# Optimization experiments

Hardware: AMD Instinct MI355X
Metric: run time of the kernel (lower is better)

## Reference

```python
import jax, jax.numpy as jnp
import numpy as np
import math

N_NODES = 20000
N_EDGES = 320000
DIM = 256
NUM_HEADS = 8


def setup_inputs() -> dict:
    key = jax.random.key(0)
    ks = jax.random.split(key, 8)
    x = jax.random.normal(ks[0], (N_NODES, DIM), dtype=jnp.float32)
    edge_index = jax.random.randint(ks[1], (2, N_EDGES), 0, N_NODES, dtype=jnp.int64)
    edge_attr = jax.random.normal(ks[2], (N_EDGES, DIM), dtype=jnp.float32)
    s = 1.0 / math.sqrt(DIM)
    Wq = jax.random.uniform(ks[3], (DIM, DIM), jnp.float32, -s, s)
    Wk = jax.random.uniform(ks[4], (DIM, DIM), jnp.float32, -s, s)
    Wv = jax.random.uniform(ks[5], (DIM, DIM), jnp.float32, -s, s)
    We = jax.random.uniform(ks[6], (DIM, DIM), jnp.float32, -s, s)
    be = jax.random.uniform(ks[7], (DIM,), jnp.float32, -s, s)
    return {"x": x, "edge_index": edge_index, "edge_attr": edge_attr,
            "Wq": Wq, "Wk": Wk, "Wv": Wv, "We": We, "be": be}


def reference(x, edge_index, edge_attr, Wq, Wk, Wv, We, be):
    N = x.shape[0]
    E = edge_attr.shape[0]
    H = NUM_HEADS
    C = DIM // H  # per-head channels (concat=True)
    src = edge_index[0]  # segment / attention-grouping index
    dst = edge_index[1]
    # Z = edge_attr * x[dst]  -> [E, D]
    Z = edge_attr * x[dst]
    q = x @ Wq.T          # [N, D]
    k = Z @ Wk.T          # [E, D]
    v = Z @ Wv.T          # [E, D]
    edge_out = Z @ We.T + be  # [E, D]
    # split heads
    qh = q.reshape(N, H, C)
    kh = k.reshape(E, H, C)
    vh = v.reshape(E, H, C)
    # per-edge, per-head score: sum(q[src]*k)/sqrt(C)   -> [E, H]
    scores = jnp.einsum('ehc,ehc->eh', qh[src], kh) / math.sqrt(C)
    # segment softmax grouped by src node
    m = jax.ops.segment_max(scores, src, num_segments=N)        # [N, H]
    ex = jnp.exp(scores - m[src])                               # [E, H]
    denom = jax.ops.segment_sum(ex, src, num_segments=N)        # [N, H]
    attn = ex / (denom[src] + 1e-16)                            # [E, H]
    # weighted scatter-sum of values -> [N, H, C] -> [N, D]
    out = jax.ops.segment_sum(attn[:, :, None] * vh, src, num_segments=N)
    out = out.reshape(N, H * C)
    return (out, edge_out)
```

## Files before the change

### kernel.cpp

```cpp
#include <hip/hip_runtime.h>
#include <math.h>

#define NN 20000
#define NE 320000
#define DIM 256

typedef __bf16 bf16x8 __attribute__((ext_vector_type(8)));
typedef float f32x4 __attribute__((ext_vector_type(4)));
typedef int i32x4 __attribute__((ext_vector_type(4)));
typedef unsigned short u16x4 __attribute__((ext_vector_type(4)));

union B8 { i32x4 i; bf16x8 b; };

__device__ __forceinline__ unsigned short f2bf(float f) {
  unsigned int u; __builtin_memcpy(&u, &f, 4);
  u += 0x7fffu + ((u >> 16) & 1u);
  return (unsigned short)(u >> 16);
}
__device__ __forceinline__ float bf2f(unsigned short h) {
  unsigned int u = ((unsigned int)h) << 16;
  float f; __builtin_memcpy(&f, &u, 4);
  return f;
}

__global__ __launch_bounds__(256) void pack_w(const float* __restrict__ W,
                                              unsigned short* __restrict__ wf) {
  int t = blockIdx.x * 256 + threadIdx.x;
  int lane = t & 63, ct = (t >> 6) & 15, ks = t >> 10;
  int col = ct * 16 + (lane & 15);
  int k0 = ks * 32 + (lane >> 4) * 8;
  const float* src = W + col * 256 + k0;
  unsigned int h[8];
#pragma unroll
  for (int j = 0; j < 8; j++) h[j] = f2bf(src[j]);
  i32x4 v;
  v.x = (int)(h[0] | (h[1] << 16));
  v.y = (int)(h[2] | (h[3] << 16));
  v.z = (int)(h[4] | (h[5] << 16));
  v.w = (int)(h[6] | (h[7] << 16));
  ((i32x4*)wf)[t] = v;
}

__device__ __forceinline__ void gemm_tile(const unsigned short* zs,
                                          const unsigned short* wf,
                                          int lane, int wv, f32x4 (&acc)[4][4]) {
#pragma unroll 1
  for (int ksI = 0; ksI < 8; ksI++) {
    bf16x8 afr[4], bfr[4];
#pragma unroll
    for (int rt = 0; rt < 4; rt++) {
      int row = rt * 16 + (lane & 15);
      int k = ksI * 32 + (lane >> 4) * 8;
      int byteo = (row * 512 + k * 2) ^ ((row & 7) << 4);
      B8 u; u.i = *(const i32x4*)((const char*)zs + byteo);
      afr[rt] = u.b;
    }
#pragma unroll
    for (int ct = 0; ct < 4; ct++) {
      B8 u; u.i = ((const i32x4*)wf)[ksI * 1024 + (wv * 4 + ct) * 64 + lane];
      bfr[ct] = u.b;
    }
#pragma unroll
    for (int rt = 0; rt < 4; rt++)
#pragma unroll
      for (int ct = 0; ct < 4; ct++)
        acc[rt][ct] = __builtin_amdgcn_mfma_f32_16x16x32_bf16(afr[rt], bfr[ct], acc[rt][ct], 0, 0, 0);
  }
}

__global__ __launch_bounds__(256) void q_kernel(const float* __restrict__ x,
                                                const unsigned short* __restrict__ wf,
                                                float* __restrict__ q) {
  __shared__ unsigned short zs[64 * 256];
  int tid = threadIdx.x, lane = tid & 63, wv = tid >> 6;
  int r0 = blockIdx.x * 64;
  int dcol = lane * 4;
#pragma unroll 4
  for (int rr = 0; rr < 16; rr++) {
    int r = rr * 4 + wv;
    int row = r0 + r;
    f32x4 a = {0.f, 0.f, 0.f, 0.f};
    if (row < NN) a = *(const f32x4*)(x + (size_t)row * DIM + dcol);
    u16x4 z;
    z.x = f2bf(a.x); z.y = f2bf(a.y); z.z = f2bf(a.z); z.w = f2bf(a.w);
    int byteo = (r * 512 + dcol * 2) ^ ((r & 7) << 4);
    *(u16x4*)((char*)zs + byteo) = z;
  }
  __syncthreads();
  f32x4 acc[4][4];
#pragma unroll
  for (int rt = 0; rt < 4; rt++)
#pragma unroll
    for (int ct = 0; ct < 4; ct++) acc[rt][ct] = (f32x4){0.f, 0.f, 0.f, 0.f};
  gemm_tile(zs, wf, lane, wv, acc);
  int cq = lane & 15, rq = lane >> 4;
#pragma unroll
  for (int ct = 0; ct < 4; ct++) {
    int col = wv * 64 + ct * 16 + cq;
#pragma unroll
    for (int rt = 0; rt < 4; rt++) {
#pragma unroll
      for (int j = 0; j < 4; j++) {
        int row = r0 + rt * 16 + rq * 4 + j;
        if (row < NN) q[(size_t)row * DIM + col] = acc[rt][ct][j];
      }
    }
  }
}

__global__ __launch_bounds__(512) void edge_kernel(
    const float* __restrict__ x, const int* __restrict__ ei,
    const float* __restrict__ ea,
    const unsigned short* __restrict__ wfk, const unsigned short* __restrict__ wfv,
    const unsigned short* __restrict__ wfe, const float* __restrict__ be,
    const float* __restrict__ q, unsigned short* __restrict__ vws,
    float* __restrict__ scores, float* __restrict__ edge_out) {
  __shared__ unsigned short zs[128 * 256];
  int tid = threadIdx.x, lane = tid & 63, wv = tid >> 6;
  int wm = wv >> 2, wn = wv & 3;
  int rq = lane >> 4, cl = lane & 15;
  int e0 = blockIdx.x * 128;

#pragma unroll
  for (int i = 0; i < 16; i++) {
    int r = i * 8 + wv;
    int dst = ei[NE + e0 + r];
    f32x4 a = *(const f32x4*)(ea + (size_t)(e0 + r) * DIM + lane * 4);
    f32x4 b = *(const f32x4*)(x + (size_t)dst * DIM + lane * 4);
    u16x4 z;
    z.x = f2bf(a.x * b.x); z.y = f2bf(a.y * b.y);
    z.z = f2bf(a.z * b.z); z.w = f2bf(a.w * b.w);
    int byteo = (r * 512 + lane * 8) ^ ((r & 7) << 4);
    *(u16x4*)((char*)zs + byteo) = z;
  }
  __syncthreads();

  const unsigned short* wfs[3] = {wfv, wfe, wfk};
  i32x4 wbuf[4][4];
  i32x4 zbuf[2][4];
  f32x4 acc[4][4];

#define LOADW(S, SLOT)                                                         \
  {                                                                            \
    const unsigned short* wfp = wfs[(S) >> 3];                                 \
    _Pragma("unroll") for (int a = 0; a < 4; a++)                              \
        wbuf[SLOT][a] =                                                        \
            ((const i32x4*)wfp)[((S) & 7) * 1024 + (wn * 4 + a) * 64 + lane];  \
  }
#define LOADZ(S, SLOT)                                                         \
  {                                                                            \
    _Pragma("unroll") for (int b = 0; b < 4; b++) {                            \
      int row = wm * 64 + b * 16 + cl;                                         \
      int kk = ((S) & 7) * 32 + rq * 8;                                        \
      int byteo = (row * 512 + kk * 2) ^ ((row & 7) << 4);                     \
      zbuf[SLOT][b] = *(const i32x4*)((const char*)zs + byteo);                \
    }                                                                          \
  }
#define GEMM_PASS(P)                                                           \
  _Pragma("unroll") for (int a = 0; a < 4; a++)                                \
      _Pragma("unroll") for (int b = 0; b < 4; b++)                            \
          acc[a][b] = (f32x4){0.f, 0.f, 0.f, 0.f};                             \
  _Pragma("unroll") for (int ks = 0; ks < 8; ks++) {                           \
    const int step = (P) * 8 + ks;                                             \
    if (step + 2 < 24) LOADW(step + 2, (step + 2) & 3);                        \
    if (step + 1 < 24) LOADZ(step + 1, (step + 1) & 1);                        \
    _Pragma("unroll") for (int a = 0; a < 4; a++) {                            \
      B8 w; w.i = wbuf[step & 3][a];                                           \
      _Pragma("unroll") for (int b = 0; b < 4; b++) {                          \
        B8 z; z.i = zbuf[step & 1][b];                                         \
        acc[a][b] = __builtin_amdgcn_mfma_f32_16x16x32_bf16(w.b, z.b,          \
                                                            acc[a][b], 0, 0, 0); \
      }                                                                        \
    }                                                                          \
  }

  LOADW(0, 0); LOADW(1, 1);
  LOADZ(0, 0); LOADZ(1, 1);

  GEMM_PASS(0)
#pragma unroll
  for (int a = 0; a < 4; a++) {
    int ch = wn * 64 + a * 16 + rq * 4;
#pragma unroll
    for (int b = 0; b < 4; b++) {
      int edge = wm * 64 + b * 16 + cl;
      u16x4 o;
      o.x = f2bf(acc[a][b][0]); o.y = f2bf(acc[a][b][1]);
      o.z = f2bf(acc[a][b][2]); o.w = f2bf(acc[a][b][3]);
      *(u16x4*)(vws + (size_t)(e0 + edge) * DIM + ch) = o;
    }
  }

  GEMM_PASS(1)
#pragma unroll
  for (int a = 0; a < 4; a++) {
    int ch = wn * 64 + a * 16 + rq * 4;
    f32x4 bias = *(const f32x4*)(be + ch);
#pragma unroll
    for (int b = 0; b < 4; b++) {
      int edge = wm * 64 + b * 16 + cl;
      f32x4 o = acc[a][b] + bias;
      *(f32x4*)(edge_out + (size_t)(e0 + edge) * DIM + ch) = o;
    }
  }

  GEMM_PASS(2)
#pragma unroll
  for (int b = 0; b < 4; b++) {
    int edge = wm * 64 + b * 16 + cl;
    int sr = ei[e0 + edge];
    const float* qp = q + (size_t)sr * DIM + wn * 64 + rq * 4;
    f32x4 q0 = *(const f32x4*)(qp);
    f32x4 q1 = *(const f32x4*)(qp + 16);
    f32x4 q2 = *(const f32x4*)(qp + 32);
    f32x4 q3 = *(const f32x4*)(qp + 48);
    float s0 = acc[0][b][0] * q0[0] + acc[0][b][1] * q0[1] +
               acc[0][b][2] * q0[2] + acc[0][b][3] * q0[3] +
               acc[1][b][0] * q1[0] + acc[1][b][1] * q1[1] +
               acc[1][b][2] * q1[2] + acc[1][b][3] * q1[3];
    float s1 = acc[2][b][0] * q2[0] + acc[2][b][1] * q2[1] +
               acc[2][b][2] * q2[2] + acc[2][b][3] * q2[3] +
               acc[3][b][0] * q3[0] + acc[3][b][1] * q3[1] +
               acc[3][b][2] * q3[2] + acc[3][b][3] * q3[3];
    s0 += __shfl_xor(s0, 16); s0 += __shfl_xor(s0, 32);
    s1 += __shfl_xor(s1, 16); s1 += __shfl_xor(s1, 32);
    if (lane < 16) {
      scores[(size_t)(e0 + edge) * 8 + wn * 2 + 0] = s0 * 0.17677669529663687f;
      scores[(size_t)(e0 + edge) * 8 + wn * 2 + 1] = s1 * 0.17677669529663687f;
    }
  }
#undef LOADW
#undef LOADZ
#undef GEMM_PASS
}

__global__ __launch_bounds__(256) void count_kernel(const int* __restrict__ ei,
                                                    int* __restrict__ counts) {
  int e = blockIdx.x * 256 + threadIdx.x;
  if (e < NE) atomicAdd(&counts[ei[e]], 1);
}

__global__ __launch_bounds__(256) void scan_kernel(const int* __restrict__ counts,
                                                   int* __restrict__ offs,
                                                   int* __restrict__ cursor) {
  __shared__ int tmp[256];
  __shared__ int carry;
  int tid = threadIdx.x;
  if (tid == 0) carry = 0;
  __syncthreads();
  for (int base = 0; base < NN; base += 256) {
    int i = base + tid;
    int v = (i < NN) ? counts[i] : 0;
    tmp[tid] = v;
    __syncthreads();
    for (int off = 1; off < 256; off <<= 1) {
      int t = (tid >= off) ? tmp[tid - off] : 0;
      __syncthreads();
      tmp[tid] += t;
      __syncthreads();
    }
    int incl = tmp[tid];
    int c0 = carry;
    if (i < NN) {
      offs[i] = c0 + incl - v;
      cursor[i] = c0 + incl - v;
    }
    __syncthreads();
    if (tid == 255) carry = c0 + incl;
    __syncthreads();
  }
  if (tid == 0) offs[NN] = carry;
}

__global__ __launch_bounds__(256) void fill_kernel(const int* __restrict__ ei,
                                                   int* __restrict__ cursor,
                                                   int* __restrict__ eids) {
  int e = blockIdx.x * 256 + threadIdx.x;
  if (e < NE) {
    int pos = atomicAdd(&cursor[ei[e]], 1);
    eids[pos] = e;
  }
}

__global__ __launch_bounds__(256) void node_kernel(const int* __restrict__ offs,
                                                   const int* __restrict__ eids,
                                                   const float* __restrict__ scores,
                                                   const unsigned short* __restrict__ vws,
                                                   float* __restrict__ out) {
  int tid = threadIdx.x;
  int n = blockIdx.x * 4 + (tid >> 6);
  int lane = tid & 63, h = lane >> 3;
  int o0 = offs[n], deg = offs[n + 1] - o0;
  float m = -INFINITY, s = 0.f;
  float a0 = 0.f, a1 = 0.f, a2 = 0.f, a3 = 0.f;
  for (int i = 0; i < deg; i++) {
    int e = eids[o0 + i];
    float sc = scores[(size_t)e * 8 + h];
    float mn = fmaxf(m, sc);
    float scale = __expf(m - mn);
    float p = __expf(sc - mn);
    s = s * scale + p;
    m = mn;
    u16x4 v = *(const u16x4*)(vws + (size_t)e * DIM + lane * 4);
    a0 = a0 * scale + p * bf2f(v.x);
    a1 = a1 * scale + p * bf2f(v.y);
    a2 = a2 * scale + p * bf2f(v.z);
    a3 = a3 * scale + p * bf2f(v.w);
  }
  float inv = 1.f / (s + 1e-16f);
  f32x4 o;
  o.x = a0 * inv; o.y = a1 * inv; o.z = a2 * inv; o.w = a3 * inv;
  *(f32x4*)(out + (size_t)n * DIM + lane * 4) = o;
}

extern "C" void kernel_launch(void* const* d_in, const int* in_sizes, int n_in,
                              void* d_out, int out_size, void* d_ws, size_t ws_size,
                              hipStream_t stream) {
  const float* x = (const float*)d_in[0];
  const int* ei = (const int*)d_in[1];
  const float* ea = (const float*)d_in[2];
  const float* Wq = (const float*)d_in[3];
  const float* Wk = (const float*)d_in[4];
  const float* Wv = (const float*)d_in[5];
  const float* We = (const float*)d_in[6];
  const float* be = (const float*)d_in[7];

  float* out = (float*)d_out;
  float* edge_out = out + (size_t)NN * DIM;
  float* q = out;
  char* ws = (char*)d_ws;
  unsigned short* wfq = (unsigned short*)(ws + 0);
  unsigned short* wfk = (unsigned short*)(ws + 131072);
  unsigned short* wfv = (unsigned short*)(ws + 262144);
  unsigned short* wfe = (unsigned short*)(ws + 393216);
  unsigned short* vws = (unsigned short*)(ws + 524288);
  float* scores = (float*)(ws + 524288 + 163840000);
  int* counts = (int*)(ws + 524288 + 163840000 + 10240000);
  int* offs = (int*)(ws + 524288 + 163840000 + 10240000 + 80000);
  int* cursor = (int*)(ws + 524288 + 163840000 + 10240000 + 160016);
  int* eids = (int*)(ws + 524288 + 163840000 + 10240000 + 240016);

  hipMemsetAsync(counts, 0, NN * sizeof(int), stream);

  pack_w<<<32, 256, 0, stream>>>(Wq, wfq);
  pack_w<<<32, 256, 0, stream>>>(Wk, wfk);
  pack_w<<<32, 256, 0, stream>>>(Wv, wfv);
  pack_w<<<32, 256, 0, stream>>>(We, wfe);

  q_kernel<<<(NN + 63) / 64, 256, 0, stream>>>(x, wfq, q);
  edge_kernel<<<NE / 128, 512, 0, stream>>>(x, ei, ea, wfk, wfv, wfe, be, q,
                                            vws, scores, edge_out);

  count_kernel<<<(NE + 255) / 256, 256, 0, stream>>>(ei, counts);
  scan_kernel<<<1, 256, 0, stream>>>(counts, offs, cursor);
  fill_kernel<<<(NE + 255) / 256, 256, 0, stream>>>(ei, cursor, eids);

  node_kernel<<<NN / 4, 256, 0, stream>>>(offs, eids, scores, vws, out);
}
```

Measured before the change: 613.6 us.

## Precompute bf16 Z, stage it via async LDS loads, and store scores in CSR order

Moves the gather-multiply that builds Z = edge_attr * x[dst] into a separate zprep kernel. It writes bf16 Z into the edge_out buffer as scratch. The GEMM kernel then fills shared memory with global_load_lds direct copies, overlapped with the first weight loads, instead of computing Z inline. The fill kernel also records each edge's CSR position, so scores are written permuted and the node kernel reads them contiguously; the node kernel additionally prefetches the next value row. The trade is an extra write and read of a 164MB bf16 Z buffer, plus a launch-bounds occupancy hint that may constrain registers.

```diff
diff --git a/kernel.cpp b/kernel.cpp
--- a/kernel.cpp
+++ b/kernel.cpp
@@ -22,6 +22,11 @@
   float f; __builtin_memcpy(&f, &u, 4);
   return f;
 }
+
+#define GLOAD16(gp, lp)                                                        \
+  __builtin_amdgcn_global_load_lds(                                            \
+      (const __attribute__((address_space(1))) unsigned int*)(gp),             \
+      (__attribute__((address_space(3))) unsigned int*)(lp), 16, 0, 0)
 
 __global__ __launch_bounds__(256) void pack_w(const float* __restrict__ W,
                                               unsigned short* __restrict__ wf) {
@@ -39,6 +44,32 @@
   v.z = (int)(h[4] | (h[5] << 16));
   v.w = (int)(h[6] | (h[7] << 16));
   ((i32x4*)wf)[t] = v;
+}
+
+__global__ __launch_bounds__(256) void zprep(const float* __restrict__ x,
+                                             const int* __restrict__ ei,
+                                             const float* __restrict__ ea,
+                                             unsigned short* __restrict__ zg) {
+  int idx = blockIdx.x * 256 + threadIdx.x;
+  int e = idx >> 4, c = idx & 15;
+  int dst = ei[NE + e];
+  const f32x4* ap = (const f32x4*)(ea + (size_t)e * DIM + c * 16);
+  const f32x4* xp = (const f32x4*)(x + (size_t)dst * DIM + c * 16);
+  unsigned int h[16];
+#pragma unroll
+  for (int j = 0; j < 4; j++) {
+    f32x4 a = ap[j], b = xp[j];
+    f32x4 p = a * b;
+    h[j * 4 + 0] = f2bf(p.x); h[j * 4 + 1] = f2bf(p.y);
+    h[j * 4 + 2] = f2bf(p.z); h[j * 4 + 3] = f2bf(p.w);
+  }
+  i32x4 o0, o1;
+  o0.x = (int)(h[0] | (h[1] << 16));  o0.y = (int)(h[2] | (h[3] << 16));
+  o0.z = (int)(h[4] | (h[5] << 16));  o0.w = (int)(h[6] | (h[7] << 16));
+  o1.x = (int)(h[8] | (h[9] << 16));  o1.y = (int)(h[10] | (h[11] << 16));
+  o1.z = (int)(h[12] | (h[13] << 16)); o1.w = (int)(h[14] | (h[15] << 16));
+  i32x4* dp = (i32x4*)(zg + (size_t)e * 512 + c * 16);
+  dp[0] = o0; dp[1] = o1;
 }
 
 __device__ __forceinline__ void gemm_tile(const unsigned short* zs,
@@ -108,32 +139,18 @@
   }
 }
 
-__global__ __launch_bounds__(512) void edge_kernel(
-    const float* __restrict__ x, const int* __restrict__ ei,
-    const float* __restrict__ ea,
+__global__ __launch_bounds__(512, 4) void gemm_edge(
+    const unsigned short* __restrict__ zg, const int* __restrict__ ei,
+    const int* __restrict__ pos,
     const unsigned short* __restrict__ wfk, const unsigned short* __restrict__ wfv,
     const unsigned short* __restrict__ wfe, const float* __restrict__ be,
     const float* __restrict__ q, unsigned short* __restrict__ vws,
-    float* __restrict__ scores, float* __restrict__ edge_out) {
+    float* __restrict__ sperm, float* __restrict__ edge_out) {
   __shared__ unsigned short zs[128 * 256];
   int tid = threadIdx.x, lane = tid & 63, wv = tid >> 6;
   int wm = wv >> 2, wn = wv & 3;
   int rq = lane >> 4, cl = lane & 15;
   int e0 = blockIdx.x * 128;
-
-#pragma unroll
-  for (int i = 0; i < 16; i++) {
-    int r = i * 8 + wv;
-    int dst = ei[NE + e0 + r];
-    f32x4 a = *(const f32x4*)(ea + (size_t)(e0 + r) * DIM + lane * 4);
-    f32x4 b = *(const f32x4*)(x + (size_t)dst * DIM + lane * 4);
-    u16x4 z;
-    z.x = f2bf(a.x * b.x); z.y = f2bf(a.y * b.y);
-    z.z = f2bf(a.z * b.z); z.w = f2bf(a.w * b.w);
-    int byteo = (r * 512 + lane * 8) ^ ((r & 7) << 4);
-    *(u16x4*)((char*)zs + byteo) = z;
-  }
-  __syncthreads();
 
   const unsigned short* wfs[3] = {wfv, wfe, wfk};
   i32x4 wbuf[4][4];
@@ -174,7 +191,19 @@
     }                                                                          \
   }
 
+  {
+    int rl = wv * 2 + (lane >> 5);
+    int c = lane & 31;
+#pragma unroll
+    for (int s = 0; s < 8; s++) {
+      int r = s * 16 + rl;
+      const unsigned short* gp = zg + (size_t)(e0 + r) * 512 + ((c ^ (r & 7)) * 8);
+      unsigned short* lp = zs + (s * 16 + wv * 2) * 256;
+      GLOAD16(gp, lp);
+    }
+  }
   LOADW(0, 0); LOADW(1, 1);
+  __syncthreads();
   LOADZ(0, 0); LOADZ(1, 1);
 
   GEMM_PASS(0)
@@ -209,6 +238,7 @@
   for (int b = 0; b < 4; b++) {
     int edge = wm * 64 + b * 16 + cl;
     int sr = ei[e0 + edge];
+    int pe = pos[e0 + edge];
     const float* qp = q + (size_t)sr * DIM + wn * 64 + rq * 4;
     f32x4 q0 = *(const f32x4*)(qp);
     f32x4 q1 = *(const f32x4*)(qp + 16);
@@ -225,8 +255,8 @@
     s0 += __shfl_xor(s0, 16); s0 += __shfl_xor(s0, 32);
     s1 += __shfl_xor(s1, 16); s1 += __shfl_xor(s1, 32);
     if (lane < 16) {
-      scores[(size_t)(e0 + edge) * 8 + wn * 2 + 0] = s0 * 0.17677669529663687f;
-      scores[(size_t)(e0 + edge) * 8 + wn * 2 + 1] = s1 * 0.17677669529663687f;
+      sperm[(size_t)pe * 8 + wn * 2 + 0] = s0 * 0.17677669529663687f;
+      sperm[(size_t)pe * 8 + wn * 2 + 1] = s1 * 0.17677669529663687f;
     }
   }
 #undef LOADW
@@ -274,17 +304,19 @@
 
 __global__ __launch_bounds__(256) void fill_kernel(const int* __restrict__ ei,
                                                    int* __restrict__ cursor,
-                                                   int* __restrict__ eids) {
+                                                   int* __restrict__ eids,
+                                                   int* __restrict__ pos) {
   int e = blockIdx.x * 256 + threadIdx.x;
   if (e < NE) {
-    int pos = atomicAdd(&cursor[ei[e]], 1);
-    eids[pos] = e;
+    int p = atomicAdd(&cursor[ei[e]], 1);
+    eids[p] = e;
+    pos[e] = p;
   }
 }
 
 __global__ __launch_bounds__(256) void node_kernel(const int* __restrict__ offs,
                                                    const int* __restrict__ eids,
-                                                   const float* __restrict__ scores,
+                                                   const float* __restrict__ sperm,
                                                    const unsigned short* __restrict__ vws,
                                                    float* __restrict__ out) {
   int tid = threadIdx.x;
@@ -293,19 +325,22 @@
   int o0 = offs[n], deg = offs[n + 1] - o0;
   float m = -INFINITY, s = 0.f;
   float a0 = 0.f, a1 = 0.f, a2 = 0.f, a3 = 0.f;
+  int e = (deg > 0) ? eids[o0] : 0;
+  u16x4 v = *(const u16x4*)(vws + (size_t)e * DIM + lane * 4);
   for (int i = 0; i < deg; i++) {
-    int e = eids[o0 + i];
-    float sc = scores[(size_t)e * 8 + h];
+    int en = (i + 1 < deg) ? eids[o0 + i + 1] : e;
+    u16x4 vn = *(const u16x4*)(vws + (size_t)en * DIM + lane * 4);
+    float sc = sperm[(size_t)(o0 + i) * 8 + h];
     float mn = fmaxf(m, sc);
     float scale = __expf(m - mn);
     float p = __expf(sc - mn);
     s = s * scale + p;
     m = mn;
-    u16x4 v = *(const u16x4*)(vws + (size_t)e * DIM + lane * 4);
     a0 = a0 * scale + p * bf2f(v.x);
     a1 = a1 * scale + p * bf2f(v.y);
     a2 = a2 * scale + p * bf2f(v.z);
     a3 = a3 * scale + p * bf2f(v.w);
+    v = vn;
   }
   float inv = 1.f / (s + 1e-16f);
   f32x4 o;
@@ -327,18 +362,21 @@
 
   float* out = (float*)d_out;
   float* edge_out = out + (size_t)NN * DIM;
+  unsigned short* zg = (unsigned short*)edge_out;
   float* q = out;
+
   char* ws = (char*)d_ws;
   unsigned short* wfq = (unsigned short*)(ws + 0);
   unsigned short* wfk = (unsigned short*)(ws + 131072);
   unsigned short* wfv = (unsigned short*)(ws + 262144);
   unsigned short* wfe = (unsigned short*)(ws + 393216);
   unsigned short* vws = (unsigned short*)(ws + 524288);
-  float* scores = (float*)(ws + 524288 + 163840000);
+  float* sperm = (float*)(ws + 524288 + 163840000);
   int* counts = (int*)(ws + 524288 + 163840000 + 10240000);
-  int* offs = (int*)(ws + 524288 + 163840000 + 10240000 + 80000);
+  int* offs   = (int*)(ws + 524288 + 163840000 + 10240000 + 80000);
   int* cursor = (int*)(ws + 524288 + 163840000 + 10240000 + 160016);
-  int* eids = (int*)(ws + 524288 + 163840000 + 10240000 + 240016);
+  int* eids   = (int*)(ws + 524288 + 163840000 + 10240000 + 240016);
+  int* pos    = (int*)(ws + 524288 + 163840000 + 10240000 + 240016 + 1280000);
 
   hipMemsetAsync(counts, 0, NN * sizeof(int), stream);
 
@@ -347,13 +385,16 @@
   pack_w<<<32, 256, 0, stream>>>(Wv, wfv);
   pack_w<<<32, 256, 0, stream>>>(We, wfe);
 
-  q_kernel<<<(NN + 63) / 64, 256, 0, stream>>>(x, wfq, q);
-  edge_kernel<<<NE / 128, 512, 0, stream>>>(x, ei, ea, wfk, wfv, wfe, be, q,
-                                            vws, scores, edge_out);
+  zprep<<<NE / 16, 256, 0, stream>>>(x, ei, ea, zg);
 
   count_kernel<<<(NE + 255) / 256, 256, 0, stream>>>(ei, counts);
   scan_kernel<<<1, 256, 0, stream>>>(counts, offs, cursor);
-  fill_kernel<<<(NE + 255) / 256, 256, 0, stream>>>(ei, cursor, eids);
-
-  node_kernel<<<NN / 4, 256, 0, stream>>>(offs, eids, scores, vws, out);
-}
+  fill_kernel<<<(NE + 255) / 256, 256, 0, stream>>>(ei, cursor, eids, pos);
+
+  q_kernel<<<(NN + 63) / 64, 256, 0, stream>>>(x, wfq, q);
+
+  gemm_edge<<<NE / 128, 512, 0, stream>>>(zg, ei, pos, wfk, wfv, wfe, be, q,
+                                          vws, sperm, edge_out);
+
+  node_kernel<<<NN / 4, 256, 0, stream>>>(offs, eids, sperm, vws, out);
+}
```

After: 1.750 ms. 185% more time.
